# Kernel optimization log

Measured on AMD Instinct MI355X. Metric: run time of the kernel, lower is better.

## Reference

```python
import jax, jax.numpy as jnp
import numpy as np

HEAD_DIM = 128
KS = 3          # kernel_size
DIL = 1         # dilation
SCALE = HEAD_DIM ** (-0.5)  # qk_scale defaults to head_dim**-0.5


def _unfold(x, ks, dil):
    # Equivalent of nn.Unfold(ks, dil, pad=dil*(ks-1)//2, stride=1), reshaped to
    # [B, d, ks*ks, H, W] (torch's C-major-then-kernel ordering matches stacking
    # kernel offsets on a new axis after the channel axis).
    B, d, H, W = x.shape
    p = dil * (ks - 1) // 2
    xp = jnp.pad(x, ((0, 0), (0, 0), (p, p), (p, p)))
    patches = [xp[:, :, i * dil:i * dil + H, j * dil:j * dil + W]
               for i in range(ks) for j in range(ks)]
    return jnp.stack(patches, axis=2)  # [B, d, ks*ks, H, W]


def setup_inputs() -> dict:
    key = jax.random.key(0)
    k1, k2, k3 = jax.random.split(key, 3)
    shape = (32, HEAD_DIM, 64, 64)
    return {
        "q": jax.random.normal(k1, shape, dtype=jnp.float32),
        "k": jax.random.normal(k2, shape, dtype=jnp.float32),
        "v": jax.random.normal(k3, shape, dtype=jnp.float32),
    }


def reference(q, k, v):
    # Local (unfold) branch: dilation=1 < 5.
    kk = _unfold(k, KS, DIL)                                   # [B,d,9,H,W]
    logits = jnp.einsum('bdhw,bdkhw->bkhw', q, kk) * SCALE     # per-pixel q @ k_window
    attn = jax.nn.softmax(logits, axis=1)                      # softmax over 9 neighbors
    vv = _unfold(v, KS, DIL)                                   # [B,d,9,H,W]
    x = jnp.einsum('bkhw,bdkhw->bhwd', attn, vv)               # [B,H,W,d]
    return x
```

## Files before the change

### kernel.cpp

```cpp
#include <hip/hip_runtime.h>
#include <hip/hip_fp16.h>

static constexpr int HD   = 128;
static constexpr int HH   = 64;
static constexpr int WW   = 64;
static constexpr int ROWS = 2;
static constexpr int BLK  = 512;
static constexpr int HALO = ROWS + 2;
static constexpr int DC   = 16;
static constexpr int NCH  = HD / DC;
static constexpr int PSTR = 8;
static constexpr float SCALE = 0.08838834764831845f;

static __device__ __forceinline__ unsigned int pkh(float a, float b) {
  __half2 h = __floats2half2_rn(a, b);
  return *(unsigned int*)&h;
}

__global__ __launch_bounds__(BLK, 4) void natten3_kernel(
    const float* __restrict__ Q, const float* __restrict__ K,
    const float* __restrict__ V, float* __restrict__ O)
{
  __shared__ unsigned int buf[2][HALO * WW * PSTR];

  const int tid = threadIdx.x;
  const int qf  = tid & 3;
  const int px  = tid >> 2;
  const int w   = px & 63;
  const int pr  = px >> 6;

  const int bid = blockIdx.x;
  const int swz = (bid & 7) * 128 + (bid >> 3);
  const int b   = swz >> 5;
  const int h0  = (swz & 31) * ROWS;
  const int hh  = h0 + pr;

  const int plane = HH * WW;
  const size_t img = (size_t)HD * plane;
  const float* Qb = Q + (size_t)b * img;
  const float* Kb = K + (size_t)b * img;
  const float* Vb = V + (size_t)b * img;
  const int qoff = hh * WW + w;
  const int dq   = 4 * qf;

  const int ws    = tid & 63;
  const int rest  = tid >> 6;
  const int is    = rest >> 1;
  const int hg    = rest & 1;
  const int grow  = min(max(h0 - 1 + is, 0), HH - 1);
  const int sgg   = grow * WW + ws;
  const int sglu  = (is * WW + ws) * PSTR + 4 * (hg ^ ((ws >> 3) & 1));
  const bool sswp = (ws >> 2) & 1;
  const int dstg  = hg * 8;

  int   lofs[9];
  float msk[9];
  #pragma unroll
  for (int dh = 0; dh < 3; ++dh) {
    #pragma unroll
    for (int dw = 0; dw < 3; ++dw) {
      const int j = dh * 3 + dw;
      const int r = hh + dh - 1, c = w + dw - 1;
      msk[j] = (r >= 0 && r < HH && c >= 0 && c < WW) ? 1.0f : 0.0f;
      const int cc = min(max(c, 0), WW - 1);
      lofs[j] = ((pr + dh) * WW + cc) * PSTR + 2 * (qf ^ ((cc >> 2) & 3));
    }
  }

  {
    float s[8];
    #pragma unroll
    for (int p = 0; p < 8; ++p) s[p] = Kb[(dstg + p) * plane + sgg];
    const unsigned int ua = pkh(s[0], s[1]), ub = pkh(s[2], s[3]);
    const unsigned int uc = pkh(s[4], s[5]), ud = pkh(s[6], s[7]);
    *(uint4*)&buf[0][sglu] = sswp ? make_uint4(uc, ud, ua, ub)
                                  : make_uint4(ua, ub, uc, ud);
  }
  float q[4];
  #pragma unroll
  for (int p = 0; p < 4; ++p) q[p] = Qb[(dq + p) * plane + qoff];
  __syncthreads();

  float logit[9];
  #pragma unroll
  for (int j = 0; j < 9; ++j) logit[j] = 0.0f;

  for (int c = 0; c < NCH; ++c) {
    const int cur = c & 1;
    float s[8], qn[4];
    if (c + 1 < NCH) {
      const int dbase = (c + 1) * DC * plane;
      #pragma unroll
      for (int p = 0; p < 8; ++p) s[p] = Kb[dbase + (dstg + p) * plane + sgg];
      #pragma unroll
      for (int p = 0; p < 4; ++p)
        qn[p] = Qb[((c + 1) * DC + dq + p) * plane + qoff];
    }
    const unsigned int* __restrict__ bc = buf[cur];
    #pragma unroll
    for (int j = 0; j < 9; ++j) {
      const uint2 r = *(const uint2*)&bc[lofs[j]];
      const float2 f01 = __half22float2(*(const __half2*)&r.x);
      const float2 f23 = __half22float2(*(const __half2*)&r.y);
      float acc = logit[j];
      acc = fmaf(q[0], f01.x, acc); acc = fmaf(q[1], f01.y, acc);
      acc = fmaf(q[2], f23.x, acc); acc = fmaf(q[3], f23.y, acc);
      logit[j] = acc;
    }
    if (c + 1 < NCH) {
      const unsigned int ua = pkh(s[0], s[1]), ub = pkh(s[2], s[3]);
      const unsigned int uc = pkh(s[4], s[5]), ud = pkh(s[6], s[7]);
      *(uint4*)&buf[cur ^ 1][sglu] = sswp ? make_uint4(uc, ud, ua, ub)
                                          : make_uint4(ua, ub, uc, ud);
      #pragma unroll
      for (int p = 0; p < 4; ++p) q[p] = qn[p];
    }
    __syncthreads();
  }

  float vs[8];
  #pragma unroll
  for (int p = 0; p < 8; ++p) vs[p] = Vb[(dstg + p) * plane + sgg];

  #pragma unroll
  for (int j = 0; j < 9; ++j) {
    logit[j] += __shfl_xor(logit[j], 1);
    logit[j] += __shfl_xor(logit[j], 2);
  }
  #pragma unroll
  for (int j = 0; j < 9; ++j) logit[j] = msk[j] * logit[j] * SCALE;
  float m = logit[0];
  #pragma unroll
  for (int j = 1; j < 9; ++j) m = fmaxf(m, logit[j]);
  float att[9];
  float Z = 0.0f;
  #pragma unroll
  for (int j = 0; j < 9; ++j) { att[j] = __expf(logit[j] - m); Z += att[j]; }
  const float rZ = 1.0f / Z;
  #pragma unroll
  for (int j = 0; j < 9; ++j) att[j] *= rZ * msk[j];

  {
    const unsigned int ua = pkh(vs[0], vs[1]), ub = pkh(vs[2], vs[3]);
    const unsigned int uc = pkh(vs[4], vs[5]), ud = pkh(vs[6], vs[7]);
    *(uint4*)&buf[0][sglu] = sswp ? make_uint4(uc, ud, ua, ub)
                                  : make_uint4(ua, ub, uc, ud);
  }
  __syncthreads();

  const size_t obase = ((size_t)b * plane + (size_t)h0 * WW) * HD;
  float oprev[4];
  for (int c = 0; c < NCH; ++c) {
    const int cur = c & 1;
    float s[8];
    if (c + 1 < NCH) {
      const int dbase = (c + 1) * DC * plane;
      #pragma unroll
      for (int p = 0; p < 8; ++p) s[p] = Vb[dbase + (dstg + p) * plane + sgg];
    }
    float o0 = 0.f, o1 = 0.f, o2 = 0.f, o3 = 0.f;
    const unsigned int* __restrict__ bc = buf[cur];
    #pragma unroll
    for (int j = 0; j < 9; ++j) {
      const uint2 r = *(const uint2*)&bc[lofs[j]];
      const float2 f01 = __half22float2(*(const __half2*)&r.x);
      const float2 f23 = __half22float2(*(const __half2*)&r.y);
      const float a = att[j];
      o0 = fmaf(a, f01.x, o0); o1 = fmaf(a, f01.y, o1);
      o2 = fmaf(a, f23.x, o2); o3 = fmaf(a, f23.y, o3);
    }
    if (c & 1) {
      const size_t oa = obase + (size_t)px * HD + (size_t)(c - 1) * DC + dq;
      *(float4*)&O[oa]      = make_float4(oprev[0], oprev[1], oprev[2], oprev[3]);
      *(float4*)&O[oa + DC] = make_float4(o0, o1, o2, o3);
    } else {
      oprev[0] = o0; oprev[1] = o1; oprev[2] = o2; oprev[3] = o3;
    }
    if (c + 1 < NCH) {
      const unsigned int ua = pkh(s[0], s[1]), ub = pkh(s[2], s[3]);
      const unsigned int uc = pkh(s[4], s[5]), ud = pkh(s[6], s[7]);
      *(uint4*)&buf[cur ^ 1][sglu] = sswp ? make_uint4(uc, ud, ua, ub)
                                          : make_uint4(ua, ub, uc, ud);
      __syncthreads();
    }
  }
}

extern "C" void kernel_launch(void* const* d_in, const int* in_sizes, int n_in,
                              void* d_out, int out_size, void* d_ws, size_t ws_size,
                              hipStream_t stream) {
  const float* q = (const float*)d_in[0];
  const float* k = (const float*)d_in[1];
  const float* v = (const float*)d_in[2];
  float* o = (float*)d_out;
  const int nblocks = 32 * (HH / ROWS);
  natten3_kernel<<<dim3(nblocks), dim3(BLK), 0, stream>>>(q, k, v, o);
}
```

Before: 45.14 us.

## Stage K/V tiles with async global_load_lds into a triple-buffered fp32 LDS pipeline

K and V chunks are now copied straight from global memory into LDS with global_load_lds instead of passing through registers and being packed to fp16. A three-slot ring buffer plus explicit vmcnt waits and raw barriers keeps two chunks in flight, and the K and V phases become one continuous 16-stage pipeline. The tiles stay fp32 in a channel-major layout padded to stride 66. This removes register staging, the conversion ALU work and a sync per iteration. In exchange it uses more LDS, which may limit occupancy, and it depends on hand-counted waitcnt values being correct.

```diff
diff --git a/kernel.cpp b/kernel.cpp
--- a/kernel.cpp
+++ b/kernel.cpp
@@ -1,5 +1,4 @@
 #include <hip/hip_runtime.h>
-#include <hip/hip_fp16.h>
 
 static constexpr int HD   = 128;
 static constexpr int HH   = 64;
@@ -9,25 +8,27 @@
 static constexpr int HALO = ROWS + 2;
 static constexpr int DC   = 16;
 static constexpr int NCH  = HD / DC;
-static constexpr int PSTR = 8;
+static constexpr int NT   = 16;
+static constexpr int PSTR = 66;
+static constexpr int SLOT = HALO * DC * PSTR;
 static constexpr float SCALE = 0.08838834764831845f;
 
-static __device__ __forceinline__ unsigned int pkh(float a, float b) {
-  __half2 h = __floats2half2_rn(a, b);
-  return *(unsigned int*)&h;
-}
+#define MEMFENCE asm volatile("" ::: "memory")
+#define VMWAIT(N) asm volatile("s_waitcnt vmcnt(" #N ")" ::: "memory")
 
 __global__ __launch_bounds__(BLK, 4) void natten3_kernel(
     const float* __restrict__ Q, const float* __restrict__ K,
     const float* __restrict__ V, float* __restrict__ O)
 {
-  __shared__ unsigned int buf[2][HALO * WW * PSTR];
-
-  const int tid = threadIdx.x;
-  const int qf  = tid & 3;
-  const int px  = tid >> 2;
-  const int w   = px & 63;
-  const int pr  = px >> 6;
+  __shared__ float buf[3][SLOT];
+
+  const int tid  = threadIdx.x;
+  const int lane = tid & 63;
+  const int wid  = tid >> 6;
+  const int qf   = tid & 3;
+  const int px   = tid >> 2;
+  const int w    = px & 63;
+  const int pr   = px >> 6;
 
   const int bid = blockIdx.x;
   const int swz = (bid & 7) * 128 + (bid >> 3);
@@ -43,146 +44,148 @@
   const int qoff = hh * WW + w;
   const int dq   = 4 * qf;
 
-  const int ws    = tid & 63;
-  const int rest  = tid >> 6;
-  const int is    = rest >> 1;
-  const int hg    = rest & 1;
-  const int grow  = min(max(h0 - 1 + is, 0), HH - 1);
-  const int sgg   = grow * WW + ws;
-  const int sglu  = (is * WW + ws) * PSTR + 4 * (hg ^ ((ws >> 3) & 1));
-  const bool sswp = (ws >> 2) & 1;
-  const int dstg  = hg * 8;
-
-  int   lofs[9];
-  float msk[9];
-  #pragma unroll
-  for (int dh = 0; dh < 3; ++dh) {
+  int gofs[8];
+  #pragma unroll
+  for (int k = 0; k < 8; ++k) {
+    const int idx = wid * 8 + k, is = idx >> 4, p = idx & 15;
+    const int grow = min(max(h0 - 1 + is, 0), HH - 1);
+    gofs[k] = p * plane + grow * WW + lane;
+  }
+  const int lbase = wid * 8 * PSTR;
+
+  int lofs[9];
+  #pragma unroll
+  for (int dh = 0; dh < 3; ++dh)
     #pragma unroll
     for (int dw = 0; dw < 3; ++dw) {
-      const int j = dh * 3 + dw;
-      const int r = hh + dh - 1, c = w + dw - 1;
-      msk[j] = (r >= 0 && r < HH && c >= 0 && c < WW) ? 1.0f : 0.0f;
-      const int cc = min(max(c, 0), WW - 1);
-      lofs[j] = ((pr + dh) * WW + cc) * PSTR + 2 * (qf ^ ((cc >> 2) & 3));
-    }
-  }
-
-  {
-    float s[8];
-    #pragma unroll
-    for (int p = 0; p < 8; ++p) s[p] = Kb[(dstg + p) * plane + sgg];
-    const unsigned int ua = pkh(s[0], s[1]), ub = pkh(s[2], s[3]);
-    const unsigned int uc = pkh(s[4], s[5]), ud = pkh(s[6], s[7]);
-    *(uint4*)&buf[0][sglu] = sswp ? make_uint4(uc, ud, ua, ub)
-                                  : make_uint4(ua, ub, uc, ud);
-  }
+      const int cc = min(max(w + dw - 1, 0), WW - 1);
+      lofs[dh * 3 + dw] = ((pr + dh) * DC + dq) * PSTR + cc;
+    }
+
+  auto STAGE = [&](int t) {
+    const float* cb = (t < NCH ? Kb : Vb) + ((t & 7) * DC) * plane;
+    float* sb = &buf[t % 3][lbase];
+    #pragma unroll
+    for (int k = 0; k < 8; ++k) {
+      __builtin_amdgcn_global_load_lds(
+          (const __attribute__((address_space(1))) void*)(cb + gofs[k]),
+          (__attribute__((address_space(3))) void*)(sb + k * PSTR), 4, 0, 0);
+    }
+  };
+
+  STAGE(0);
   float q[4];
   #pragma unroll
   for (int p = 0; p < 4; ++p) q[p] = Qb[(dq + p) * plane + qoff];
-  __syncthreads();
+  MEMFENCE;
+  STAGE(1);
 
   float logit[9];
   #pragma unroll
   for (int j = 0; j < 9; ++j) logit[j] = 0.0f;
 
+  #pragma unroll 1
   for (int c = 0; c < NCH; ++c) {
-    const int cur = c & 1;
-    float s[8], qn[4];
+    VMWAIT(12);
+    __builtin_amdgcn_s_barrier();
+    MEMFENCE;
+    float qn[4];
     if (c + 1 < NCH) {
-      const int dbase = (c + 1) * DC * plane;
-      #pragma unroll
-      for (int p = 0; p < 8; ++p) s[p] = Kb[dbase + (dstg + p) * plane + sgg];
       #pragma unroll
       for (int p = 0; p < 4; ++p)
         qn[p] = Qb[((c + 1) * DC + dq + p) * plane + qoff];
     }
-    const unsigned int* __restrict__ bc = buf[cur];
+    MEMFENCE;
+    STAGE(c + 2);
+    const float* __restrict__ bc = &buf[c % 3][0];
     #pragma unroll
     for (int j = 0; j < 9; ++j) {
-      const uint2 r = *(const uint2*)&bc[lofs[j]];
-      const float2 f01 = __half22float2(*(const __half2*)&r.x);
-      const float2 f23 = __half22float2(*(const __half2*)&r.y);
       float acc = logit[j];
-      acc = fmaf(q[0], f01.x, acc); acc = fmaf(q[1], f01.y, acc);
-      acc = fmaf(q[2], f23.x, acc); acc = fmaf(q[3], f23.y, acc);
+      acc = fmaf(q[0], bc[lofs[j]], acc);
+      acc = fmaf(q[1], bc[lofs[j] + PSTR], acc);
+      acc = fmaf(q[2], bc[lofs[j] + 2 * PSTR], acc);
+      acc = fmaf(q[3], bc[lofs[j] + 3 * PSTR], acc);
       logit[j] = acc;
     }
     if (c + 1 < NCH) {
-      const unsigned int ua = pkh(s[0], s[1]), ub = pkh(s[2], s[3]);
-      const unsigned int uc = pkh(s[4], s[5]), ud = pkh(s[6], s[7]);
-      *(uint4*)&buf[cur ^ 1][sglu] = sswp ? make_uint4(uc, ud, ua, ub)
-                                          : make_uint4(ua, ub, uc, ud);
       #pragma unroll
       for (int p = 0; p < 4; ++p) q[p] = qn[p];
     }
-    __syncthreads();
-  }
-
-  float vs[8];
-  #pragma unroll
-  for (int p = 0; p < 8; ++p) vs[p] = Vb[(dstg + p) * plane + sgg];
+  }
 
   #pragma unroll
   for (int j = 0; j < 9; ++j) {
     logit[j] += __shfl_xor(logit[j], 1);
     logit[j] += __shfl_xor(logit[j], 2);
   }
-  #pragma unroll
-  for (int j = 0; j < 9; ++j) logit[j] = msk[j] * logit[j] * SCALE;
-  float m = logit[0];
-  #pragma unroll
-  for (int j = 1; j < 9; ++j) m = fmaxf(m, logit[j]);
   float att[9];
-  float Z = 0.0f;
-  #pragma unroll
-  for (int j = 0; j < 9; ++j) { att[j] = __expf(logit[j] - m); Z += att[j]; }
-  const float rZ = 1.0f / Z;
-  #pragma unroll
-  for (int j = 0; j < 9; ++j) att[j] *= rZ * msk[j];
-
   {
-    const unsigned int ua = pkh(vs[0], vs[1]), ub = pkh(vs[2], vs[3]);
-    const unsigned int uc = pkh(vs[4], vs[5]), ud = pkh(vs[6], vs[7]);
-    *(uint4*)&buf[0][sglu] = sswp ? make_uint4(uc, ud, ua, ub)
-                                  : make_uint4(ua, ub, uc, ud);
-  }
-  __syncthreads();
+    float msk[9];
+    #pragma unroll
+    for (int dh = 0; dh < 3; ++dh)
+      #pragma unroll
+      for (int dw = 0; dw < 3; ++dw) {
+        const int j = dh * 3 + dw;
+        const int r = hh + dh - 1, c = w + dw - 1;
+        msk[j] = (r >= 0 && r < HH && c >= 0 && c < WW) ? 1.0f : 0.0f;
+      }
+    #pragma unroll
+    for (int j = 0; j < 9; ++j) logit[j] = msk[j] * logit[j] * SCALE;
+    float m = logit[0];
+    #pragma unroll
+    for (int j = 1; j < 9; ++j) m = fmaxf(m, logit[j]);
+    float Z = 0.0f;
+    #pragma unroll
+    for (int j = 0; j < 9; ++j) { att[j] = __expf(logit[j] - m); Z += att[j]; }
+    const float rZ = 1.0f / Z;
+    #pragma unroll
+    for (int j = 0; j < 9; ++j) att[j] *= rZ * msk[j];
+  }
 
   const size_t obase = ((size_t)b * plane + (size_t)h0 * WW) * HD;
   float oprev[4];
-  for (int c = 0; c < NCH; ++c) {
-    const int cur = c & 1;
-    float s[8];
-    if (c + 1 < NCH) {
-      const int dbase = (c + 1) * DC * plane;
-      #pragma unroll
-      for (int p = 0; p < 8; ++p) s[p] = Vb[dbase + (dstg + p) * plane + sgg];
-    }
+  #pragma unroll 1
+  for (int t = NCH; t < NT - 1; ++t) {
+    VMWAIT(8);
+    __builtin_amdgcn_s_barrier();
+    MEMFENCE;
+    if (t + 2 < NT) STAGE(t + 2);
+    const float* __restrict__ bc = &buf[t % 3][0];
     float o0 = 0.f, o1 = 0.f, o2 = 0.f, o3 = 0.f;
-    const unsigned int* __restrict__ bc = buf[cur];
     #pragma unroll
     for (int j = 0; j < 9; ++j) {
-      const uint2 r = *(const uint2*)&bc[lofs[j]];
-      const float2 f01 = __half22float2(*(const __half2*)&r.x);
-      const float2 f23 = __half22float2(*(const __half2*)&r.y);
       const float a = att[j];
-      o0 = fmaf(a, f01.x, o0); o1 = fmaf(a, f01.y, o1);
-      o2 = fmaf(a, f23.x, o2); o3 = fmaf(a, f23.y, o3);
-    }
-    if (c & 1) {
-      const size_t oa = obase + (size_t)px * HD + (size_t)(c - 1) * DC + dq;
+      o0 = fmaf(a, bc[lofs[j]], o0);
+      o1 = fmaf(a, bc[lofs[j] + PSTR], o1);
+      o2 = fmaf(a, bc[lofs[j] + 2 * PSTR], o2);
+      o3 = fmaf(a, bc[lofs[j] + 3 * PSTR], o3);
+    }
+    const int lc = t - NCH;
+    if (lc & 1) {
+      const size_t oa = obase + (size_t)px * HD + (size_t)(lc - 1) * DC + dq;
       *(float4*)&O[oa]      = make_float4(oprev[0], oprev[1], oprev[2], oprev[3]);
       *(float4*)&O[oa + DC] = make_float4(o0, o1, o2, o3);
     } else {
       oprev[0] = o0; oprev[1] = o1; oprev[2] = o2; oprev[3] = o3;
     }
-    if (c + 1 < NCH) {
-      const unsigned int ua = pkh(s[0], s[1]), ub = pkh(s[2], s[3]);
-      const unsigned int uc = pkh(s[4], s[5]), ud = pkh(s[6], s[7]);
-      *(uint4*)&buf[cur ^ 1][sglu] = sswp ? make_uint4(uc, ud, ua, ub)
-                                          : make_uint4(ua, ub, uc, ud);
-      __syncthreads();
-    }
+  }
+  {
+    VMWAIT(0);
+    __builtin_amdgcn_s_barrier();
+    MEMFENCE;
+    const float* __restrict__ bc = &buf[(NT - 1) % 3][0];
+    float o0 = 0.f, o1 = 0.f, o2 = 0.f, o3 = 0.f;
+    #pragma unroll
+    for (int j = 0; j < 9; ++j) {
+      const float a = att[j];
+      o0 = fmaf(a, bc[lofs[j]], o0);
+      o1 = fmaf(a, bc[lofs[j] + PSTR], o1);
+      o2 = fmaf(a, bc[lofs[j] + 2 * PSTR], o2);
+      o3 = fmaf(a, bc[lofs[j] + 3 * PSTR], o3);
+    }
+    const size_t oa = obase + (size_t)px * HD + (size_t)6 * DC + dq;
+    *(float4*)&O[oa]      = make_float4(oprev[0], oprev[1], oprev[2], oprev[3]);
+    *(float4*)&O[oa + DC] = make_float4(o0, o1, o2, o3);
   }
 }
 
```

Measured after the change: 49.25 us. 9.1% more time.
